# Kernel optimization log

Measured on AMD Instinct MI355X. Metric: run time of the kernel, lower is better.

Reference implementation:

```python
import jax, jax.numpy as jnp
import numpy as np

DIM = 768
NUM_HEADS = 12
HEAD_DIM = DIM // NUM_HEADS
SCALE = HEAD_DIM ** -0.5


def setup_inputs() -> dict:
    key = jax.random.key(0)
    k1, k2, k3 = jax.random.split(key, 3)
    x = jax.random.normal(k1, (32, 577, DIM), dtype=jnp.float32)
    # torch nn.Linear weights are [out_features, in_features]
    W_qkv = jax.random.normal(k2, (3 * DIM, DIM), dtype=jnp.float32) * (DIM ** -0.5)
    W_proj = jax.random.normal(k3, (DIM, DIM), dtype=jnp.float32) * (DIM ** -0.5)
    b_proj = jnp.zeros((DIM,), dtype=jnp.float32)
    return {"x": x, "W_qkv": W_qkv, "W_proj": W_proj, "b_proj": b_proj}


def reference(x, W_qkv, W_proj, b_proj):
    B, N, C = x.shape
    H, D = NUM_HEADS, C // NUM_HEADS
    # qkv: [B, N, 3C] -> [3, B, H, N, D]
    qkv = (x @ W_qkv.T).reshape(B, N, 3, H, D).transpose(2, 0, 3, 1, 4)
    q, k, v = qkv[0], qkv[1], qkv[2]
    attn = jnp.einsum('bhnd,bhmd->bhnm', q, k) * SCALE
    attn = jax.nn.softmax(attn, axis=-1)
    out = jnp.einsum('bhnm,bhmd->bhnd', attn, v)  # [B, H, N, D]
    out = out.transpose(0, 2, 1, 3).reshape(B, N, C)
    return out @ W_proj.T + b_proj
```

## Files before the change

### kernel.cpp

```cpp
#include <hip/hip_runtime.h>
#include <math.h>

#define SEQ    577
#define BATCH  32
#define DIM    768
#define NHEAD  12
#define HDIM   64
#define MROWS  (BATCH * SEQ)
#define QKVN   (3 * DIM)

using half4   = __attribute__((ext_vector_type(4))) _Float16;
using half8   = __attribute__((ext_vector_type(8))) _Float16;
using floatx4 = __attribute__((ext_vector_type(4))) float;

typedef __attribute__((address_space(1))) const unsigned int GU;
typedef __attribute__((address_space(3))) unsigned int LU;

__device__ __forceinline__ void gld_lds16(const _Float16* g, _Float16* l) {
    __builtin_amdgcn_global_load_lds((const GU*)g, (LU*)l, 16, 0, 0);
}

__device__ __forceinline__ unsigned lds_addr(const void* p) {
    return (unsigned)(size_t)(LU*)p;
}

__global__ void cvt3_f32_f16(const float* __restrict__ a, _Float16* __restrict__ ao, int na4,
                             const float* __restrict__ b, _Float16* __restrict__ bo, int nb4,
                             const float* __restrict__ c, _Float16* __restrict__ co, int nc4)
{
    int i = blockIdx.x * blockDim.x + threadIdx.x;
    int stride = gridDim.x * blockDim.x;
    int total = na4 + nb4 + nc4;
    for (; i < total; i += stride) {
        const float4* src; half4* dst; int j = i;
        if (j < na4)            { src = (const float4*)a; dst = (half4*)ao; }
        else if ((j -= na4) < nb4) { src = (const float4*)b; dst = (half4*)bo; }
        else { j -= nb4;          src = (const float4*)c; dst = (half4*)co; }
        float4 v = src[j];
        half4 h;
        h[0] = (_Float16)v.x; h[1] = (_Float16)v.y;
        h[2] = (_Float16)v.z; h[3] = (_Float16)v.w;
        dst[j] = h;
    }
}

template<int OUT_HALF, int HAS_BIAS, int SCALEQ>
__global__ __launch_bounds__(256) void gemm_f16_lds(
    const _Float16* __restrict__ A, const _Float16* __restrict__ B,
    const float* __restrict__ bias, void* __restrict__ Cp,
    int M, int N, int K, int npm, int npn)
{
    __shared__ _Float16 As[2][2 * 128 * 32];
    __shared__ _Float16 Bs[2][2 * 128 * 32];

    const int GROUP = 8;
    int pid  = blockIdx.x;
    int ngrp = GROUP * npn;
    int g    = pid / ngrp;
    int fm   = g * GROUP;
    int gm   = npm - fm; if (gm > GROUP) gm = GROUP;
    int pm   = fm + (pid % ngrp) % gm;
    int pn   = (pid % ngrp) / gm;
    const int m0 = pm * 128, n0 = pn * 128;

    const int t    = threadIdx.x, lane = t & 63, wv = t >> 6;
    const int quad = lane >> 4,   ln   = lane & 15;
    const int wm   = wv >> 1,     wn   = wv & 1;

    floatx4 acc[4][4];
#pragma unroll
    for (int mt = 0; mt < 4; mt++)
#pragma unroll
        for (int nt = 0; nt < 4; nt++) acc[mt][nt] = {0.f, 0.f, 0.f, 0.f};

    const int sr  = wv * 32 + (lane >> 2);
    const int scl = (lane & 3) * 8;
    const int scg = ((lane & 3) ^ ((lane >> 3) & 3)) * 8;
    int ma0 = m0 + sr;      if (ma0 > M - 1) ma0 = M - 1;
    int ma1 = m0 + sr + 16; if (ma1 > M - 1) ma1 = M - 1;
    const _Float16* Ag0 = A + (size_t)ma0 * K + scg;
    const _Float16* Ag1 = A + (size_t)ma1 * K + scg;
    const _Float16* Bg0 = B + (size_t)(n0 + sr) * K + scg;
    const _Float16* Bg1 = B + (size_t)(n0 + sr + 16) * K + scg;
    const int PHALF = 128 * 32;
    const int l0 = sr * 32 + scl;
    const int l1 = (sr + 16) * 32 + scl;

    const int nk = K >> 6;

#pragma unroll
    for (int p = 0; p < 2; p++) {
        gld_lds16(Ag0 + p * 32, &As[0][l0 + p * PHALF]);
        gld_lds16(Ag1 + p * 32, &As[0][l1 + p * PHALF]);
        gld_lds16(Bg0 + p * 32, &Bs[0][l0 + p * PHALF]);
        gld_lds16(Bg1 + p * 32, &Bs[0][l1 + p * PHALF]);
    }

    const int rq = (ln >> 1) & 3;

    for (int it = 0; it < nk; it++) {
        const int cur = it & 1;

        __syncthreads();

        if (it + 1 < nk) {
            const int kn = (it + 1) << 6, nb = cur ^ 1;
#pragma unroll
            for (int p = 0; p < 2; p++) {
                gld_lds16(Ag0 + kn + p * 32, &As[nb][l0 + p * PHALF]);
                gld_lds16(Ag1 + kn + p * 32, &As[nb][l1 + p * PHALF]);
                gld_lds16(Bg0 + kn + p * 32, &Bs[nb][l0 + p * PHALF]);
                gld_lds16(Bg1 + kn + p * 32, &Bs[nb][l1 + p * PHALF]);
            }
        }
        __builtin_amdgcn_sched_barrier(0);

#pragma unroll
        for (int p = 0; p < 2; p++) {
            half8 af[4], bf[4];
#pragma unroll
            for (int mt = 0; mt < 4; mt++)
                af[mt] = *(const half8*)&As[cur][p * PHALF + (wm * 64 + mt * 16 + ln) * 32 + ((quad ^ rq) << 3)];
#pragma unroll
            for (int nt = 0; nt < 4; nt++)
                bf[nt] = *(const half8*)&Bs[cur][p * PHALF + (wn * 64 + nt * 16 + ln) * 32 + ((quad ^ rq) << 3)];
#pragma unroll
            for (int mt = 0; mt < 4; mt++)
#pragma unroll
                for (int nt = 0; nt < 4; nt++)
                    acc[mt][nt] = __builtin_amdgcn_mfma_f32_16x16x32_f16(
                        af[mt], bf[nt], acc[mt][nt], 0, 0, 0);
        }
    }

    float bv[4];
    if constexpr (HAS_BIAS) {
#pragma unroll
        for (int nt = 0; nt < 4; nt++) bv[nt] = bias[n0 + wn * 64 + nt * 16 + ln];
    }
    float*    C32 = (float*)Cp;
    _Float16* C16 = (_Float16*)Cp;
#pragma unroll
    for (int mt = 0; mt < 4; mt++)
#pragma unroll
        for (int r = 0; r < 4; r++) {
            int m = m0 + wm * 64 + mt * 16 + quad * 4 + r;
            if (m < M) {
#pragma unroll
                for (int nt = 0; nt < 4; nt++) {
                    int col = n0 + wn * 64 + nt * 16 + ln;
                    float v = acc[mt][nt][r];
                    if constexpr (HAS_BIAS) v += bv[nt];
                    if constexpr (SCALEQ) { if (col < DIM) v *= 0.18033688f; }
                    if constexpr (OUT_HALF) C16[(size_t)m * N + col] = (_Float16)v;
                    else                    C32[(size_t)m * N + col] = v;
                }
            }
        }
}

__global__ __launch_bounds__(256) void attn_f16(
    const _Float16* __restrict__ qkv, _Float16* __restrict__ outp)
{
    __shared__ _Float16 Ks[2][64 * 64];
    __shared__ _Float16 Vs[2][64 * 64];

    const int t    = threadIdx.x, lane = t & 63, wv = t >> 6;
    const int quad = lane >> 4,   ln   = lane & 15;
    const int q0   = blockIdx.x * 128;
    const int hd   = blockIdx.y,  b    = blockIdx.z;
    const _Float16* base = qkv + (size_t)b * SEQ * QKVN;

    half8 qreg[2][2];
#pragma unroll
    for (int qc = 0; qc < 2; qc++) {
        int q = q0 + wv * 32 + qc * 16 + ln; if (q >= SEQ) q = SEQ - 1;
#pragma unroll
        for (int kd = 0; kd < 2; kd++)
            qreg[qc][kd] = *(const half8*)(base + (size_t)q * QKVN + hd * HDIM + kd * 32 + quad * 8);
    }

    const int krow = t >> 3;
    const int kdc  = (t & 7) ^ (krow & 7);
    const int vkey = ((t >> 7) << 4) + (((t >> 3) & 3) << 2) + ((t >> 1) & 3);
    const int vd0  = (((t >> 5) & 3) << 4) + ((t & 1) << 3);
    const _Float16* kcst = base + DIM     + hd * HDIM + kdc * 8;
    const _Float16* vcst = base + 2 * DIM + hd * HDIM + vd0;

    float lr[2] = {0.f, 0.f};
    floatx4 o[2][4];
#pragma unroll
    for (int qc = 0; qc < 2; qc++)
#pragma unroll
        for (int dt = 0; dt < 4; dt++) o[qc][dt] = {0.f, 0.f, 0.f, 0.f};

    const unsigned vb0 = lds_addr(&Vs[0][0]) + lane * 8;

    gld_lds16(kcst + (size_t)krow * QKVN,        &Ks[0][t * 8]);
    gld_lds16(kcst + (size_t)(krow + 32) * QKVN, &Ks[0][(t + 256) * 8]);
    gld_lds16(vcst + (size_t)vkey * QKVN,        &Vs[0][t * 8]);
    gld_lds16(vcst + (size_t)(vkey + 32) * QKVN, &Vs[0][(t + 256) * 8]);

    for (int kt0 = 0; kt0 < 10; kt0++) {
        const int cur = kt0 & 1;
        const int k0  = kt0 * 64;

        __syncthreads();

        if (kt0 < 9) {
            const int k1 = k0 + 64, nb = cur ^ 1;
            int r0 = k1 + krow;      if (r0 > SEQ - 1) r0 = SEQ - 1;
            int r1 = k1 + krow + 32; if (r1 > SEQ - 1) r1 = SEQ - 1;
            int s0 = k1 + vkey;      if (s0 > SEQ - 1) s0 = SEQ - 1;
            int s1 = k1 + vkey + 32; if (s1 > SEQ - 1) s1 = SEQ - 1;
            gld_lds16(kcst + (size_t)r0 * QKVN, &Ks[nb][t * 8]);
            gld_lds16(kcst + (size_t)r1 * QKVN, &Ks[nb][(t + 256) * 8]);
            gld_lds16(vcst + (size_t)s0 * QKVN, &Vs[nb][t * 8]);
            gld_lds16(vcst + (size_t)s1 * QKVN, &Vs[nb][(t + 256) * 8]);
        }
        __builtin_amdgcn_sched_barrier(0);

        floatx4 sacc[2][4];
#pragma unroll
        for (int qc = 0; qc < 2; qc++)
#pragma unroll
            for (int mt = 0; mt < 4; mt++) sacc[qc][mt] = {0.f, 0.f, 0.f, 0.f};
        const int xr = ln & 7;
#pragma unroll
        for (int kd = 0; kd < 2; kd++) {
            half8 kf[4];
#pragma unroll
            for (int mt = 0; mt < 4; mt++)
                kf[mt] = *(const half8*)&Ks[cur][(mt * 16 + ln) * 64 + (((kd * 4 + quad) ^ xr) << 3)];
#pragma unroll
            for (int mt = 0; mt < 4; mt++) {
                sacc[0][mt] = __builtin_amdgcn_mfma_f32_16x16x32_f16(kf[mt], qreg[0][kd], sacc[0][mt], 0, 0, 0);
                sacc[1][mt] = __builtin_amdgcn_mfma_f32_16x16x32_f16(kf[mt], qreg[1][kd], sacc[1][mt], 0, 0, 0);
            }
        }

        half4 vf[4][4];
        const unsigned vb = vb0 + (cur << 13);
#pragma unroll
        for (int kt = 0; kt < 4; kt++) {
            unsigned a = vb + kt * 2048;
            asm volatile("ds_read_b64_tr_b16 %0, %1 offset:0"    : "=v"(vf[kt][0]) : "v"(a));
            asm volatile("ds_read_b64_tr_b16 %0, %1 offset:512"  : "=v"(vf[kt][1]) : "v"(a));
            asm volatile("ds_read_b64_tr_b16 %0, %1 offset:1024" : "=v"(vf[kt][2]) : "v"(a));
            asm volatile("ds_read_b64_tr_b16 %0, %1 offset:1536" : "=v"(vf[kt][3]) : "v"(a));
        }

        if (k0 + 64 > SEQ) {
#pragma unroll
            for (int mt = 0; mt < 4; mt++)
#pragma unroll
                for (int r = 0; r < 4; r++)
                    if (k0 + mt * 16 + quad * 4 + r >= SEQ) {
                        sacc[0][mt][r] = -3e38f;
                        sacc[1][mt][r] = -3e38f;
                    }
        }

        half4 pf[2][4];
#pragma unroll
        for (int qc = 0; qc < 2; qc++) {
#pragma unroll
            for (int mt = 0; mt < 4; mt++)
#pragma unroll
                for (int r = 0; r < 4; r++) {
                    float p = exp2f(sacc[qc][mt][r]);
                    lr[qc] += p;
                    pf[qc][mt][r] = (_Float16)p;
                }
        }

        asm volatile("s_waitcnt lgkmcnt(0)" ::: "memory");
        __builtin_amdgcn_sched_barrier(0);
#pragma unroll
        for (int kt = 0; kt < 4; kt++) {
#pragma unroll
            for (int dt = 0; dt < 4; dt++) {
                o[0][dt] = __builtin_amdgcn_mfma_f32_16x16x16f16(vf[kt][dt], pf[0][kt], o[0][dt], 0, 0, 0);
                o[1][dt] = __builtin_amdgcn_mfma_f32_16x16x16f16(vf[kt][dt], pf[1][kt], o[1][dt], 0, 0, 0);
            }
        }
    }

#pragma unroll
    for (int qc = 0; qc < 2; qc++) {
        lr[qc] += __shfl_xor(lr[qc], 16);
        lr[qc] += __shfl_xor(lr[qc], 32);
    }

#pragma unroll
    for (int qc = 0; qc < 2; qc++) {
        int q = q0 + wv * 32 + qc * 16 + ln;
        if (q < SEQ) {
            float inv = 1.f / lr[qc];
#pragma unroll
            for (int dt = 0; dt < 4; dt++) {
                half4 hv;
                hv[0] = (_Float16)(o[qc][dt][0] * inv);
                hv[1] = (_Float16)(o[qc][dt][1] * inv);
                hv[2] = (_Float16)(o[qc][dt][2] * inv);
                hv[3] = (_Float16)(o[qc][dt][3] * inv);
                *(half4*)&outp[(size_t)(b * SEQ + q) * DIM + hd * HDIM + dt * 16 + quad * 4] = hv;
            }
        }
    }
}

extern "C" void kernel_launch(void* const* d_in, const int* in_sizes, int n_in,
                              void* d_out, int out_size, void* d_ws, size_t ws_size,
                              hipStream_t stream)
{
    const float* x     = (const float*)d_in[0];
    const float* Wqkv  = (const float*)d_in[1];
    const float* Wproj = (const float*)d_in[2];
    const float* bproj = (const float*)d_in[3];
    float* out = (float*)d_out;

    const size_t NX  = (size_t)MROWS * DIM;
    const size_t NWQ = (size_t)QKVN * DIM;
    const size_t NWP = (size_t)DIM * DIM;

    _Float16* x16    = (_Float16*)d_ws;
    _Float16* Wq16   = x16 + NX;
    _Float16* Wp16   = Wq16 + NWQ;
    _Float16* qkv16  = Wp16 + NWP;
    _Float16* attn16 = qkv16 + (size_t)MROWS * QKVN;

    cvt3_f32_f16<<<2048, 256, 0, stream>>>(x, x16, (int)(NX / 4),
                                           Wqkv, Wq16, (int)(NWQ / 4),
                                           Wproj, Wp16, (int)(NWP / 4));

    {
        int npm = (MROWS + 127) / 128, npn = QKVN / 128;
        gemm_f16_lds<1, 0, 1><<<npm * npn, 256, 0, stream>>>(
            x16, Wq16, nullptr, qkv16, MROWS, QKVN, DIM, npm, npn);
    }

    attn_f16<<<dim3((SEQ + 127) / 128, NHEAD, BATCH), 256, 0, stream>>>(qkv16, attn16);

    {
        int npm = (MROWS + 127) / 128, npn = DIM / 128;
        gemm_f16_lds<0, 1, 0><<<npm * npn, 256, 0, stream>>>(
            attn16, Wp16, bproj, out, MROWS, DIM, DIM, npm, npn);
    }
}
```

Baseline: 344.5 us.

## Prefetch two K-tiles ahead with explicit vmcnt waits in GEMM mainloop

```diff
diff --git a/kernel.cpp b/kernel.cpp
--- a/kernel.cpp
+++ b/kernel.cpp
@@ -88,31 +88,32 @@
 
     const int nk = K >> 6;
 
-#pragma unroll
-    for (int p = 0; p < 2; p++) {
-        gld_lds16(Ag0 + p * 32, &As[0][l0 + p * PHALF]);
-        gld_lds16(Ag1 + p * 32, &As[0][l1 + p * PHALF]);
-        gld_lds16(Bg0 + p * 32, &Bs[0][l0 + p * PHALF]);
-        gld_lds16(Bg1 + p * 32, &Bs[0][l1 + p * PHALF]);
-    }
+#define STAGE_G(it, buf)                                            \
+    {                                                               \
+        const int kn_ = (it) << 6;                                  \
+        _Float16* as_ = &As[(buf)][0];                              \
+        _Float16* bs_ = &Bs[(buf)][0];                              \
+        gld_lds16(Ag0 + kn_,      as_ + l0);                        \
+        gld_lds16(Ag1 + kn_,      as_ + l1);                        \
+        gld_lds16(Bg0 + kn_,      bs_ + l0);                        \
+        gld_lds16(Bg1 + kn_,      bs_ + l1);                        \
+        gld_lds16(Ag0 + kn_ + 32, as_ + l0 + PHALF);                \
+        gld_lds16(Ag1 + kn_ + 32, as_ + l1 + PHALF);                \
+        gld_lds16(Bg0 + kn_ + 32, bs_ + l0 + PHALF);                \
+        gld_lds16(Bg1 + kn_ + 32, bs_ + l1 + PHALF);                \
+    }
+
+    STAGE_G(0, 0);
+    if (nk > 1) STAGE_G(1, 1);
 
     const int rq = (ln >> 1) & 3;
 
     for (int it = 0; it < nk; it++) {
         const int cur = it & 1;
 
-        __syncthreads();
-
-        if (it + 1 < nk) {
-            const int kn = (it + 1) << 6, nb = cur ^ 1;
-#pragma unroll
-            for (int p = 0; p < 2; p++) {
-                gld_lds16(Ag0 + kn + p * 32, &As[nb][l0 + p * PHALF]);
-                gld_lds16(Ag1 + kn + p * 32, &As[nb][l1 + p * PHALF]);
-                gld_lds16(Bg0 + kn + p * 32, &Bs[nb][l0 + p * PHALF]);
-                gld_lds16(Bg1 + kn + p * 32, &Bs[nb][l1 + p * PHALF]);
-            }
-        }
+        if (it + 1 < nk) asm volatile("s_waitcnt vmcnt(8)" ::: "memory");
+        else             asm volatile("s_waitcnt vmcnt(0)" ::: "memory");
+        __builtin_amdgcn_s_barrier();
         __builtin_amdgcn_sched_barrier(0);
 
 #pragma unroll
@@ -131,7 +132,12 @@
                     acc[mt][nt] = __builtin_amdgcn_mfma_f32_16x16x32_f16(
                         af[mt], bf[nt], acc[mt][nt], 0, 0, 0);
         }
-    }
+
+        __builtin_amdgcn_sched_barrier(0);
+        __builtin_amdgcn_s_barrier();
+        if (it + 2 < nk) STAGE_G(it + 2, cur);
+    }
+#undef STAGE_G
 
     float bv[4];
     if constexpr (HAS_BIAS) {
```

Measured after the change: 341.9 us. Within noise of the previous version (-0.8%).
